# Performance work log

Measured on AMD Instinct MI355X. Metric: run time of the kernel, lower is better.

Reference implementation:

```python
import jax, jax.numpy as jnp
import numpy as np

HIDDEN, KEY_DIM, VALUE_DIM = 1024, 1024, 1024
BATCH, SEQ = 8, 2048


def setup_inputs() -> dict:
    key = jax.random.key(0)
    ks = jax.random.split(key, 9)
    s = lambda fan_in: 1.0 / np.sqrt(fan_in)
    return {
        "y_all": jax.random.normal(ks[0], (BATCH, SEQ, HIDDEN), dtype=jnp.float32),
        # torch nn.Linear weights stored as (in, out) for x @ W + b
        "Wq": jax.random.uniform(ks[1], (HIDDEN, KEY_DIM), jnp.float32, -s(HIDDEN), s(HIDDEN)),
        "bq": jax.random.uniform(ks[2], (KEY_DIM,), jnp.float32, -s(HIDDEN), s(HIDDEN)),
        "Wk": jax.random.uniform(ks[3], (HIDDEN, KEY_DIM), jnp.float32, -s(HIDDEN), s(HIDDEN)),
        "bk": jax.random.uniform(ks[4], (KEY_DIM,), jnp.float32, -s(HIDDEN), s(HIDDEN)),
        "Wv": jax.random.uniform(ks[5], (HIDDEN, VALUE_DIM), jnp.float32, -s(HIDDEN), s(HIDDEN)),
        "bv": jax.random.uniform(ks[6], (VALUE_DIM,), jnp.float32, -s(HIDDEN), s(HIDDEN)),
        "Wo": jax.random.uniform(ks[7], (VALUE_DIM, HIDDEN), jnp.float32, -s(VALUE_DIM), s(VALUE_DIM)),
        "bo": jax.random.uniform(ks[8], (HIDDEN,), jnp.float32, -s(VALUE_DIM), s(VALUE_DIM)),
    }


def reference(y_all, Wq, bq, Wk, bk, Wv, bv, Wo, bo):
    # Original loops over t, each step attending last hidden state to the full
    # prefix. Equivalent to a single causal-masked attention pass.
    B, T, H = y_all.shape
    dk = Wq.shape[1]
    q = (y_all @ Wq + bq) / jnp.sqrt(jnp.asarray(dk, y_all.dtype))  # [B,T,dk]
    k = y_all @ Wk + bk                                              # [B,T,dk]
    v = y_all @ Wv + bv                                              # [B,T,dv]
    scores = jnp.einsum("bid,bjd->bij", q, k)                        # [B,T,T]
    causal = jnp.tril(jnp.ones((T, T), dtype=bool))                  # j <= i
    scores = jnp.where(causal, scores, -jnp.inf)
    weights = jax.nn.softmax(scores, axis=-1)
    ctx = jnp.einsum("bij,bjd->bid", weights, v)                     # [B,T,dv]
    return ctx @ Wo + bo                                             # [B,T,H]
```

## Files before the change

kernel.cpp:

```cpp
#include <hip/hip_runtime.h>

typedef __attribute__((ext_vector_type(8))) __bf16 bf16x8;
typedef __attribute__((ext_vector_type(4))) float f32x4;
typedef __attribute__((ext_vector_type(4))) float f4;
typedef __attribute__((ext_vector_type(4))) unsigned short ushort4_t;

__device__ inline void gload16(const void* g, void* l) {
  __builtin_amdgcn_global_load_lds(
      (const __attribute__((address_space(1))) unsigned int*)g,
      (__attribute__((address_space(3))) unsigned int*)l, 16, 0, 0);
}

__global__ void convert_bf16_k(const float* __restrict__ in, __bf16* __restrict__ out, int n8) {
  int i = blockIdx.x * blockDim.x + threadIdx.x;
  int stride = gridDim.x * blockDim.x;
  for (; i < n8; i += stride) {
    f4 a = ((const f4*)in)[2 * (long long)i];
    f4 b = ((const f4*)in)[2 * (long long)i + 1];
    bf16x8 o;
#pragma unroll
    for (int e = 0; e < 4; e++) { o[e] = (__bf16)a[e]; o[e + 4] = (__bf16)b[e]; }
    ((bf16x8*)out)[i] = o;
  }
}

__global__ void pack_bias_k(const float* __restrict__ bq, const float* __restrict__ bk,
                            const float* __restrict__ bv, float* __restrict__ out) {
  int i = blockIdx.x * 256 + threadIdx.x;
  if (i >= 3072) return;
  const float* src = (i < 1024) ? bq : (i < 2048) ? bk : bv;
  out[i] = src[i & 1023];
}

__global__ void transpose_w_k(const float* __restrict__ W0, const float* __restrict__ W1,
                              const float* __restrict__ W2, const float* __restrict__ W3,
                              __bf16* __restrict__ out) {
  int z = blockIdx.z;
  const float* W = (z == 0) ? W0 : (z == 1) ? W1 : (z == 2) ? W2 : W3;
  __bf16* O = out + (long long)z * 1048576;
  __shared__ float tile[32][33];
  int tx = threadIdx.x, ty = threadIdx.y;
  int n0 = blockIdx.x * 32, k0 = blockIdx.y * 32;
#pragma unroll
  for (int i = 0; i < 4; i++)
    tile[ty + i * 8][tx] = W[(long long)(k0 + ty + i * 8) * 1024 + n0 + tx];
  __syncthreads();
#pragma unroll
  for (int i = 0; i < 4; i++)
    O[(long long)(n0 + ty + i * 8) * 1024 + k0 + tx] = (__bf16)tile[tx][ty + i * 8];
}


#define ABUF(P, H) (lds + ((P) * 2 + (H)) * 8192)
#define BBUF(P, H) (lds + 32768 + ((P) * 2 + (H)) * 8192)

#define LOADA(P, MIB)                                                          \
  _Pragma("unroll") for (int mi = 0; mi < 4; mi++)                             \
      _Pragma("unroll") for (int kh = 0; kh < 2; kh++) {                       \
    int row = ((MIB) + mi) * 16 + ln15;                                        \
    int pb = (row * 128 + (kh * 32 + kq * 8) * 2) ^ ((row & 7) << 4);          \
    a[mi][kh] = *(const bf16x8*)((const char*)ABUF(P, wm) + pb);               \
  }

#define LOADB(P, NIB)                                                          \
  _Pragma("unroll") for (int ni = 0; ni < 2; ni++)                             \
      _Pragma("unroll") for (int kh = 0; kh < 2; kh++) {                       \
    int row = brow0 + ((NIB) + ni) * 16 + ln15;                                \
    int pb = (row * 128 + (kh * 32 + kq * 8) * 2) ^ ((row & 7) << 4);          \
    b[(NIB) + ni][kh] = *(const bf16x8*)((const char*)BBUF(P, bh) + pb);       \
  }

#define MFMAQ(MI0, NI0)                                                        \
  _Pragma("unroll") for (int mi = 0; mi < 4; mi++)                             \
      _Pragma("unroll") for (int ni = 0; ni < 2; ni++)                         \
          _Pragma("unroll") for (int kh = 0; kh < 2; kh++)                     \
              acc[(MI0) + mi][(NI0) + ni] =                                    \
      __builtin_amdgcn_mfma_f32_16x16x32_bf16(a[mi][kh], b[(NI0) + ni][kh],    \
                                              acc[(MI0) + mi][(NI0) + ni], 0, 0, 0);

#define FENCE asm volatile("" ::: "memory")

#define BARW                                           \
  FENCE;                                               \
  __builtin_amdgcn_s_barrier();                        \
  FENCE;                                               \
  __builtin_amdgcn_s_setprio(1);

#define ENDP                                           \
  __builtin_amdgcn_s_setprio(0);                       \
  FENCE;                                               \
  __builtin_amdgcn_s_barrier();                        \
  FENCE;

#define ENDPB                                          \
  __builtin_amdgcn_s_setprio(0);                       \
  asm volatile("s_waitcnt vmcnt(4)" ::: "memory");     \
  __builtin_amdgcn_s_barrier();                        \
  FENCE;

template <int OUT, int SWZ>
__global__ __launch_bounds__(512, 2) void gemm8(
    const __bf16* __restrict__ A0, int lda, long long sAz,
    const __bf16* __restrict__ B0, int ldb, long long sBz,
    void* __restrict__ C0v, int ldc, long long sCz,
    const float* __restrict__ bias0, int sBiasZ,
    float scale_z0, int k_tiles_base, int k_tiles_per_br,
    __bf16* __restrict__ vt_out) {
  int br, bc, z;
  {
    const int lin = (blockIdx.z * gridDim.y + blockIdx.y) * gridDim.x + blockIdx.x;
    if (SWZ == 1) {
      const int q = lin & 7, c = lin >> 3;
      br = q * 8 + (c & 7);
      bc = c >> 3;
      z = 0;
    } else if (SWZ == 2) {
      const int q = lin & 7, c = lin >> 3;
      z = q;
      int b0 = (int)((sqrtf((float)(8 * c + 1)) - 1.0f) * 0.5f);
      int c0 = c - ((b0 * (b0 + 1)) >> 1);
      if (c0 < 0) { b0--; c0 = c - ((b0 * (b0 + 1)) >> 1); }
      if (c0 > b0) { b0++; c0 = c - ((b0 * (b0 + 1)) >> 1); }
      br = b0;
      bc = c0;
    } else {
      const int nbx = gridDim.x, nby = gridDim.y;
      const int nwg = nbx * nby * gridDim.z;
      const int cpx = nwg >> 3;
      const int swz = (lin & 7) * cpx + (lin >> 3);
      br = swz % nbx;
      const int tmp = swz / nbx;
      bc = tmp % nby;
      z = tmp / nby;
    }
  }
  const int kt = k_tiles_base + k_tiles_per_br * br;

  __shared__ __align__(16) __bf16 lds[65536];

  const int t = threadIdx.x, w = t >> 6, lane = t & 63;
  const int wm = w >> 2, wn = w & 3;
  const int ln15 = lane & 15, kq = lane >> 4;
  const int bh = wn >> 1, brow0 = (wn & 1) * 64;

  const __bf16* A = A0 + (long long)z * sAz + (long long)br * 256 * lda;
  const __bf16* B = B0 + (long long)z * sBz + (long long)bc * 256 * ldb;

  int r0s[2], c0s[2];
#pragma unroll
  for (int i = 0; i < 2; i++) {
    int o = i * 8192 + t * 16;
    int lo = o ^ (((o >> 7) & 7) << 4);
    r0s[i] = lo >> 7;
    c0s[i] = (lo & 127) >> 1;
  }
  const __bf16 *sA0[2], *sA1[2], *sB0[2], *sB1[2];
#pragma unroll
  for (int i = 0; i < 2; i++) {
    sA0[i] = A + (long long)r0s[i] * lda + c0s[i];
    sA1[i] = A + (long long)(r0s[i] + 128) * lda + c0s[i];
    sB0[i] = B + (long long)r0s[i] * ldb + c0s[i];
    sB1[i] = B + (long long)(r0s[i] + 128) * ldb + c0s[i];
  }

  auto stg = [&](const __bf16* const* src, __bf16* lbase, int ktile) {
    int kc = ktile < kt ? ktile : kt - 1;
#pragma unroll
    for (int i = 0; i < 2; i++)
      gload16(src[i] + kc * 64, lbase + i * 4096 + w * 512);
  };

  f32x4 acc[8][4] = {};
  bf16x8 a[4][2], b[4][2];

  stg(sB0, BBUF(0, 0), 0);
  stg(sB1, BBUF(0, 1), 0);
  stg(sA0, ABUF(0, 0), 0);
  stg(sA1, ABUF(0, 1), 0);
  stg(sB0, BBUF(1, 0), 1);
  stg(sB1, BBUF(1, 1), 1);
  asm volatile("s_waitcnt vmcnt(4)" ::: "memory");
  __builtin_amdgcn_s_barrier();
  FENCE;

  for (int kk = 0; kk < kt; kk += 2) {
    LOADA(0, 0) LOADB(0, 0)
    stg(sA0, ABUF(1, 0), kk + 1);
    BARW MFMAQ(0, 0) ENDP
    LOADB(0, 2)
    stg(sA1, ABUF(1, 1), kk + 1);
    BARW MFMAQ(0, 2) ENDP
    LOADA(0, 4)
    stg(sB0, BBUF(0, 0), kk + 2);
    BARW MFMAQ(4, 2) ENDP
    stg(sB1, BBUF(0, 1), kk + 2);
    BARW MFMAQ(4, 0) ENDPB
    LOADA(1, 0) LOADB(1, 0)
    stg(sA0, ABUF(0, 0), kk + 2);
    BARW MFMAQ(0, 0) ENDP
    LOADB(1, 2)
    stg(sA1, ABUF(0, 1), kk + 2);
    BARW MFMAQ(0, 2) ENDP
    LOADA(1, 4)
    stg(sB0, BBUF(1, 0), kk + 3);
    BARW MFMAQ(4, 2) ENDP
    stg(sB1, BBUF(1, 1), kk + 3);
    BARW MFMAQ(4, 0) ENDPB
  }

  const int row0 = br * 256 + wm * 128 + kq * 4;
  const int col0 = bc * 256 + wn * 64 + ln15;
  if (OUT == 2) {
#pragma unroll
    for (int mi = 0; mi < 8; mi++) {
      const int rr = row0 + mi * 16;
#pragma unroll
      for (int ni = 0; ni < 4; ni++) {
        const int cc = col0 + ni * 16;
        const float bb = bias0[cc];
        if (cc < 2048) {
          const float s = (cc < 1024) ? scale_z0 : 1.0f;
#pragma unroll
          for (int j = 0; j < 4; j++)
            ((__bf16*)C0v)[(long long)(rr + j) * ldc + cc] =
                (__bf16)((acc[mi][ni][j] + bb) * s);
        } else {
          const int d = cc - 2048, bz = rr >> 11, t0 = rr & 2047;
          ushort4_t p;
#pragma unroll
          for (int j = 0; j < 4; j++) {
            union { __bf16 h; unsigned short u; } cv;
            cv.h = (__bf16)(acc[mi][ni][j] + bb);
            p[j] = cv.u;
          }
          *(ushort4_t*)(vt_out + (long long)bz * 2097152 + (long long)d * 2048 + t0) = p;
        }
      }
    }
  } else {
    const float scale = (z == 0) ? scale_z0 : 1.0f;
    const float* bias = bias0 ? (bias0 + (long long)z * sBiasZ) : nullptr;
#pragma unroll
    for (int mi = 0; mi < 8; mi++) {
#pragma unroll
      for (int ni = 0; ni < 4; ni++) {
        const int rr = row0 + mi * 16;
        const int cc = col0 + ni * 16;
        const float bb = bias ? bias[cc] : 0.0f;
#pragma unroll
        for (int j = 0; j < 4; j++) {
          float v = (acc[mi][ni][j] + bb) * scale;
          long long off = (long long)z * sCz + (long long)(rr + j) * ldc + cc;
          if (OUT == 1)
            ((float*)C0v)[off] = v;
          else
            ((__bf16*)C0v)[off] = (__bf16)v;
        }
      }
    }
  }
}

__global__ __launch_bounds__(256) void softmax_rows(__bf16* __restrict__ S) {
  const int row = blockIdx.x;
  const int i = row & 2047;
  __bf16* s = S + (long long)row * 2048;
  const int Lpad = (i + 256) & ~255;
  const int t = threadIdx.x;
  const int j0 = t * 8;
  const int wid = t >> 6, lane = t & 63;
  const bool active = j0 < Lpad;

  float v[8];
  float mymax = -3.0e38f;
  if (active) {
    bf16x8 x = *(const bf16x8*)(s + j0);
#pragma unroll
    for (int e = 0; e < 8; e++) {
      float f = (float)x[e];
      v[e] = ((j0 + e) <= i) ? f : -3.0e38f;
      mymax = fmaxf(mymax, v[e]);
    }
  }
  float mw = mymax;
#pragma unroll
  for (int o = 32; o >= 1; o >>= 1) mw = fmaxf(mw, __shfl_xor(mw, o));
  __shared__ float redm[4];
  __shared__ float reds[4];
  if (lane == 0) redm[wid] = mw;
  __syncthreads();
  const float m = fmaxf(fmaxf(redm[0], redm[1]), fmaxf(redm[2], redm[3]));

  float e8[8];
  float mysum = 0.0f;
  if (active) {
#pragma unroll
    for (int e = 0; e < 8; e++) {
      float ev = ((j0 + e) <= i) ? __expf(v[e] - m) : 0.0f;
      e8[e] = ev;
      mysum += ev;
    }
  } else {
#pragma unroll
    for (int e = 0; e < 8; e++) e8[e] = 0.0f;
  }
  float sw = mysum;
#pragma unroll
  for (int o = 32; o >= 1; o >>= 1) sw += __shfl_xor(sw, o);
  if (lane == 0) reds[wid] = sw;
  __syncthreads();
  const float l = reds[0] + reds[1] + reds[2] + reds[3];
  const float rl = 1.0f / l;
  if (active) {
    bf16x8 o;
#pragma unroll
    for (int e = 0; e < 8; e++) o[e] = (__bf16)(e8[e] * rl);
    *(bf16x8*)(s + j0) = o;
  }
}

extern "C" void kernel_launch(void* const* d_in, const int* in_sizes, int n_in,
                              void* d_out, int out_size, void* d_ws, size_t ws_size,
                              hipStream_t stream) {
  const float* y  = (const float*)d_in[0];
  const float* Wq = (const float*)d_in[1];
  const float* bq = (const float*)d_in[2];
  const float* Wk = (const float*)d_in[3];
  const float* bk = (const float*)d_in[4];
  const float* Wv = (const float*)d_in[5];
  const float* bv = (const float*)d_in[6];
  const float* Wo = (const float*)d_in[7];
  const float* bo = (const float*)d_in[8];

  char* ws = (char*)d_ws;
  __bf16* Xb   = (__bf16*)(ws + 0);
  __bf16* Wt   = (__bf16*)(ws + 33554432);
  float*  bqkv = (float*)(ws + 41943040);
  __bf16* QK   = (__bf16*)(ws + 41955328);
  __bf16* Vt   = (__bf16*)(ws + 109064192);
  __bf16* Sb   = (__bf16*)(ws + 142618624);
  __bf16* ctx  = (__bf16*)(ws + 0);

  if (ws_size < 209727488u) return;

  convert_bf16_k<<<2048, 256, 0, stream>>>(y, Xb, 2097152);
  pack_bias_k<<<12, 256, 0, stream>>>(bq, bk, bv, bqkv);
  transpose_w_k<<<dim3(32, 32, 4), dim3(32, 8), 0, stream>>>(Wq, Wk, Wv, Wo, Wt);

  gemm8<2, 1><<<dim3(64, 12, 1), 512, 0, stream>>>(
      Xb, 1024, 0LL, Wt, 1024, 0LL,
      QK, 2048, 0LL, bqkv, 0, 0.03125f, 16, 0, Vt);

  gemm8<0, 2><<<dim3(36, 1, 8), 512, 0, stream>>>(
      QK, 2048, 4194304LL, QK + 1024, 2048, 4194304LL,
      Sb, 2048, 4194304LL, nullptr, 0, 1.0f, 16, 0, nullptr);

  softmax_rows<<<16384, 256, 0, stream>>>(Sb);

  gemm8<0, 0><<<dim3(8, 4, 8), 512, 0, stream>>>(
      Sb, 2048, 4194304LL, Vt, 2048, 2097152LL,
      ctx, 1024, 2097152LL, nullptr, 0, 1.0f, 4, 4, nullptr);

  gemm8<1, 1><<<dim3(64, 4, 1), 512, 0, stream>>>(
      ctx, 1024, 0LL, Wt + 3 * 1048576, 1024, 0LL,
      d_out, 1024, 0LL, bo, 0, 1.0f, 16, 0, nullptr);
}
```

Measured before the change: 317.3 us.

## Compute Q, K and V tiles in one block to reuse the X tile

The QKV projection GEMM now launches a third as many blocks. Each block loops over three weight segments (Q, K, V) for the same 256-row slice of X, writing Q and K after their segments and resetting the accumulators. The V output is now transposed through LDS with a swizzle so the Vt stores are coalesced 16-byte writes, replacing scattered 8-byte ones. This cuts redundant reads of X and the uncoalesced transpose stores. In exchange the grid shrinks to 256 blocks, which may leave CUs underused, and each block runs three times as long.

```diff
diff --git a/kernel.cpp b/kernel.cpp
--- a/kernel.cpp
+++ b/kernel.cpp
@@ -98,7 +98,7 @@
   __builtin_amdgcn_s_barrier();                        \
   FENCE;
 
-template <int OUT, int SWZ>
+template <int OUT, int SWZ, int NSEG>
 __global__ __launch_bounds__(512, 2) void gemm8(
     const __bf16* __restrict__ A0, int lda, long long sAz,
     const __bf16* __restrict__ B0, int ldb, long long sBz,
@@ -135,6 +135,7 @@
     }
   }
   const int kt = k_tiles_base + k_tiles_per_br * br;
+  const int ktend = kt * NSEG;
 
   __shared__ __align__(16) __bf16 lds[65536];
 
@@ -145,6 +146,7 @@
 
   const __bf16* A = A0 + (long long)z * sAz + (long long)br * 256 * lda;
   const __bf16* B = B0 + (long long)z * sBz + (long long)bc * 256 * ldb;
+  if (SWZ == 1 && NSEG > 1) B = B0 + (long long)bc * 256 * ldb;
 
   int r0s[2], c0s[2];
 #pragma unroll
@@ -163,81 +165,116 @@
     sB1[i] = B + (long long)(r0s[i] + 128) * ldb + c0s[i];
   }
 
-  auto stg = [&](const __bf16* const* src, __bf16* lbase, int ktile) {
-    int kc = ktile < kt ? ktile : kt - 1;
+  auto stg = [&](const __bf16* const* src, __bf16* lbase, int g, long long segstr) {
+    int gc = g < ktend ? g : ktend - 1;
+    int seg, kc;
+    if (NSEG > 1) { seg = gc >> 4; kc = gc & 15; }
+    else { seg = 0; kc = gc; }
 #pragma unroll
     for (int i = 0; i < 2; i++)
-      gload16(src[i] + kc * 64, lbase + i * 4096 + w * 512);
+      gload16(src[i] + (long long)seg * segstr + kc * 64, lbase + i * 4096 + w * 512);
   };
 
   f32x4 acc[8][4] = {};
   bf16x8 a[4][2], b[4][2];
 
-  stg(sB0, BBUF(0, 0), 0);
-  stg(sB1, BBUF(0, 1), 0);
-  stg(sA0, ABUF(0, 0), 0);
-  stg(sA1, ABUF(0, 1), 0);
-  stg(sB0, BBUF(1, 0), 1);
-  stg(sB1, BBUF(1, 1), 1);
+  stg(sB0, BBUF(0, 0), 0, sBz);
+  stg(sB1, BBUF(0, 1), 0, sBz);
+  stg(sA0, ABUF(0, 0), 0, 0);
+  stg(sA1, ABUF(0, 1), 0, 0);
+  stg(sB0, BBUF(1, 0), 1, sBz);
+  stg(sB1, BBUF(1, 1), 1, sBz);
   asm volatile("s_waitcnt vmcnt(4)" ::: "memory");
   __builtin_amdgcn_s_barrier();
   FENCE;
 
-  for (int kk = 0; kk < kt; kk += 2) {
-    LOADA(0, 0) LOADB(0, 0)
-    stg(sA0, ABUF(1, 0), kk + 1);
-    BARW MFMAQ(0, 0) ENDP
-    LOADB(0, 2)
-    stg(sA1, ABUF(1, 1), kk + 1);
-    BARW MFMAQ(0, 2) ENDP
-    LOADA(0, 4)
-    stg(sB0, BBUF(0, 0), kk + 2);
-    BARW MFMAQ(4, 2) ENDP
-    stg(sB1, BBUF(0, 1), kk + 2);
-    BARW MFMAQ(4, 0) ENDPB
-    LOADA(1, 0) LOADB(1, 0)
-    stg(sA0, ABUF(0, 0), kk + 2);
-    BARW MFMAQ(0, 0) ENDP
-    LOADB(1, 2)
-    stg(sA1, ABUF(0, 1), kk + 2);
-    BARW MFMAQ(0, 2) ENDP
-    LOADA(1, 4)
-    stg(sB0, BBUF(1, 0), kk + 3);
-    BARW MFMAQ(4, 2) ENDP
-    stg(sB1, BBUF(1, 1), kk + 3);
-    BARW MFMAQ(4, 0) ENDPB
-  }
-
-  const int row0 = br * 256 + wm * 128 + kq * 4;
-  const int col0 = bc * 256 + wn * 64 + ln15;
-  if (OUT == 2) {
-#pragma unroll
-    for (int mi = 0; mi < 8; mi++) {
-      const int rr = row0 + mi * 16;
-#pragma unroll
-      for (int ni = 0; ni < 4; ni++) {
-        const int cc = col0 + ni * 16;
-        const float bb = bias0[cc];
-        if (cc < 2048) {
-          const float s = (cc < 1024) ? scale_z0 : 1.0f;
+  for (int s = 0; s < NSEG; s++) {
+    for (int kk = 0; kk < kt; kk += 2) {
+      const int g = s * kt + kk;
+      LOADA(0, 0) LOADB(0, 0)
+      stg(sA0, ABUF(1, 0), g + 1, 0);
+      BARW MFMAQ(0, 0) ENDP
+      LOADB(0, 2)
+      stg(sA1, ABUF(1, 1), g + 1, 0);
+      BARW MFMAQ(0, 2) ENDP
+      LOADA(0, 4)
+      stg(sB0, BBUF(0, 0), g + 2, sBz);
+      BARW MFMAQ(4, 2) ENDP
+      stg(sB1, BBUF(0, 1), g + 2, sBz);
+      BARW MFMAQ(4, 0) ENDPB
+      LOADA(1, 0) LOADB(1, 0)
+      stg(sA0, ABUF(0, 0), g + 2, 0);
+      BARW MFMAQ(0, 0) ENDP
+      LOADB(1, 2)
+      stg(sA1, ABUF(0, 1), g + 2, 0);
+      BARW MFMAQ(0, 2) ENDP
+      LOADA(1, 4)
+      stg(sB0, BBUF(1, 0), g + 3, sBz);
+      BARW MFMAQ(4, 2) ENDP
+      stg(sB1, BBUF(1, 1), g + 3, sBz);
+      BARW MFMAQ(4, 0) ENDPB
+    }
+    if (OUT == 2 && s + 1 < NSEG) {
+      const int ccb = (bc + 4 * s) * 256 + wn * 64 + ln15;
+      const int rrb = br * 256 + wm * 128 + kq * 4;
+      const float sc = (s == 0) ? scale_z0 : 1.0f;
+#pragma unroll
+      for (int mi = 0; mi < 8; mi++) {
+#pragma unroll
+        for (int ni = 0; ni < 4; ni++) {
+          const int rr = rrb + mi * 16;
+          const int cc = ccb + ni * 16;
+          const float bb = bias0[cc];
 #pragma unroll
           for (int j = 0; j < 4; j++)
             ((__bf16*)C0v)[(long long)(rr + j) * ldc + cc] =
-                (__bf16)((acc[mi][ni][j] + bb) * s);
-        } else {
-          const int d = cc - 2048, bz = rr >> 11, t0 = rr & 2047;
-          ushort4_t p;
-#pragma unroll
-          for (int j = 0; j < 4; j++) {
-            union { __bf16 h; unsigned short u; } cv;
-            cv.h = (__bf16)(acc[mi][ni][j] + bb);
-            p[j] = cv.u;
-          }
-          *(ushort4_t*)(vt_out + (long long)bz * 2097152 + (long long)d * 2048 + t0) = p;
+                (__bf16)((acc[mi][ni][j] + bb) * sc);
+          acc[mi][ni] = (f32x4){0.0f, 0.0f, 0.0f, 0.0f};
         }
       }
     }
+  }
+
+  if (OUT == 2) {
+    __syncthreads();
+    char* lb = (char*)lds;
+    const int dl0 = wn * 64 + ln15;
+    const int tl0 = wm * 128 + kq * 4;
+#pragma unroll
+    for (int mi = 0; mi < 8; mi++) {
+#pragma unroll
+      for (int ni = 0; ni < 4; ni++) {
+        const int d = dl0 + ni * 16;
+        const int tl = tl0 + mi * 16;
+        const float bb = bias0[2048 + bc * 256 + d];
+        ushort4_t p;
+#pragma unroll
+        for (int j = 0; j < 4; j++) {
+          union { __bf16 h; unsigned short u; } cv;
+          cv.h = (__bf16)(acc[mi][ni][j] + bb);
+          p[j] = cv.u;
+        }
+        int byte = d * 512 + tl * 2;
+        byte ^= (d & 7) << 4;
+        *(ushort4_t*)(lb + byte) = p;
+      }
+    }
+    __syncthreads();
+    const int bz = br >> 3;
+    __bf16* vbase = vt_out + (long long)bz * 2097152 +
+                    (long long)(bc * 256) * 2048 + (br & 7) * 256;
+#pragma unroll
+    for (int it = 0; it < 16; it++) {
+      int idx = it * 512 + t;
+      int d = idx >> 5, tc = idx & 31;
+      int byte = d * 512 + tc * 16;
+      byte ^= (d & 7) << 4;
+      bf16x8 vv = *(const bf16x8*)(lb + byte);
+      *(bf16x8*)(vbase + (long long)d * 2048 + tc * 8) = vv;
+    }
   } else {
+    const int row0 = br * 256 + wm * 128 + kq * 4;
+    const int col0 = bc * 256 + wn * 64 + ln15;
     const float scale = (z == 0) ? scale_z0 : 1.0f;
     const float* bias = bias0 ? (bias0 + (long long)z * sBiasZ) : nullptr;
 #pragma unroll
@@ -347,21 +384,21 @@
   pack_bias_k<<<12, 256, 0, stream>>>(bq, bk, bv, bqkv);
   transpose_w_k<<<dim3(32, 32, 4), dim3(32, 8), 0, stream>>>(Wq, Wk, Wv, Wo, Wt);
 
-  gemm8<2, 1><<<dim3(64, 12, 1), 512, 0, stream>>>(
-      Xb, 1024, 0LL, Wt, 1024, 0LL,
+  gemm8<2, 1, 3><<<dim3(64, 4, 1), 512, 0, stream>>>(
+      Xb, 1024, 0LL, Wt, 1024, 1048576LL,
       QK, 2048, 0LL, bqkv, 0, 0.03125f, 16, 0, Vt);
 
-  gemm8<0, 2><<<dim3(36, 1, 8), 512, 0, stream>>>(
+  gemm8<0, 2, 1><<<dim3(36, 1, 8), 512, 0, stream>>>(
       QK, 2048, 4194304LL, QK + 1024, 2048, 4194304LL,
       Sb, 2048, 4194304LL, nullptr, 0, 1.0f, 16, 0, nullptr);
 
   softmax_rows<<<16384, 256, 0, stream>>>(Sb);
 
-  gemm8<0, 0><<<dim3(8, 4, 8), 512, 0, stream>>>(
+  gemm8<0, 0, 1><<<dim3(8, 4, 8), 512, 0, stream>>>(
       Sb, 2048, 4194304LL, Vt, 2048, 2097152LL,
       ctx, 1024, 2097152LL, nullptr, 0, 1.0f, 4, 4, nullptr);
 
-  gemm8<1, 1><<<dim3(64, 4, 1), 512, 0, stream>>>(
+  gemm8<1, 1, 1><<<dim3(64, 4, 1), 512, 0, stream>>>(
       ctx, 1024, 0LL, Wt + 3 * 1048576, 1024, 0LL,
       d_out, 1024, 0LL, bo, 0, 1.0f, 16, 0, nullptr);
 }
```

After: 334.0 us. 5.3% more time.
